# Performance work log

Hardware: AMD Instinct MI355X
Metric: run time of the kernel (lower is better)

Reference implementation:

```python
import jax, jax.numpy as jnp
import numpy as np

N = 100000
E = 3200000
IN_CH = 256
HID = 32
OUT_CH = 16


def setup_inputs() -> dict:
    key = jax.random.key(0)
    ks = jax.random.split(key, 9)
    x = jax.random.normal(ks[0], (N, IN_CH), dtype=jnp.float32)
    row = jax.random.randint(ks[1], (E,), 0, N)
    col = jax.random.randint(ks[2], (E,), 0, N)
    edge_index = jnp.stack([row, col], axis=0)  # [2, E]
    # Glorot-style init for GCN weights, zero bias (PyG default)
    def glorot(k, fan_in, fan_out):
        s = jnp.sqrt(6.0 / (fan_in + fan_out))
        return jax.random.uniform(k, (fan_in, fan_out), jnp.float32, -s, s)
    W1 = glorot(ks[3], IN_CH, HID)
    b1 = jnp.zeros((HID,), jnp.float32)
    W_mu = glorot(ks[4], HID, OUT_CH)
    b_mu = jnp.zeros((OUT_CH,), jnp.float32)
    W_lv = glorot(ks[5], HID, OUT_CH)
    b_lv = jnp.zeros((OUT_CH,), jnp.float32)
    return {"x": x, "edge_index": edge_index, "W1": W1, "b1": b1,
            "W_mu": W_mu, "b_mu": b_mu, "W_lv": W_lv, "b_lv": b_lv}


def _gcn_norm(edge_index, n):
    # PyG gcn_norm with add_self_loops=True: deg over target col including self-loop
    row, col = edge_index[0], edge_index[1]
    deg = jax.ops.segment_sum(jnp.ones((edge_index.shape[1],), jnp.float32), col,
                              num_segments=n) + 1.0  # +1 for self-loop
    dis = jax.lax.rsqrt(deg)  # deg >= 1 always
    edge_norm = dis[row] * dis[col]          # [E]
    self_norm = dis * dis                    # [N], norm of self-loop edge
    return edge_norm, self_norm


def _gcn_conv(x, W, b, row, col, edge_norm, self_norm, n):
    h = x @ W  # [N, F_out] — transform BEFORE aggregation (small F_out)
    agg = jax.ops.segment_sum(h[row] * edge_norm[:, None], col, num_segments=n)
    return agg + self_norm[:, None] * h + b


def reference(x, edge_index, W1, b1, W_mu, b_mu, W_lv, b_lv):
    n = x.shape[0]
    row, col = edge_index[0], edge_index[1]
    edge_norm, self_norm = _gcn_norm(edge_index, n)
    h = jax.nn.relu(_gcn_conv(x, W1, b1, row, col, edge_norm, self_norm, n))
    mu = _gcn_conv(h, W_mu, b_mu, row, col, edge_norm, self_norm, n)
    logvar = _gcn_conv(h, W_lv, b_lv, row, col, edge_norm, self_norm, n)
    return (mu, logvar)
```

## Files before the change

kernel.cpp:

```cpp
#include <hip/hip_runtime.h>

#define N_NODES 100000
#define E_EDGES 3200000
#define IN_CH 256
#define HID 32
#define OUT_CH 16

#define B_BUCKETS 250
#define NPB 400
#define CAP 20000
#define PB 256
#define PCH (E_EDGES / PB)
#define GEMM_BLOCKS ((N_NODES + 63) / 64)

typedef unsigned short u16;
typedef __attribute__((ext_vector_type(8))) short bf16x8;
typedef __attribute__((ext_vector_type(4))) float f32x4;

__device__ __forceinline__ unsigned bf16rtn(float f) {
    unsigned u = __float_as_uint(f);
    return (u + 0x7FFFu + ((u >> 16) & 1u)) >> 16;
}
__device__ __forceinline__ float bflo(unsigned u) { return __uint_as_float(u << 16); }
__device__ __forceinline__ float bfhi(unsigned u) { return __uint_as_float(u & 0xFFFF0000u); }


__global__ __launch_bounds__(256) void k_pre(const int* __restrict__ col,
                                             int* __restrict__ ghist,
                                             const float* __restrict__ W1,
                                             const float* __restrict__ x,
                                             u16* __restrict__ h0sh, int e, int n) {
    int bid = blockIdx.x;
    int tid = threadIdx.x;
    if (bid < PB) {
        __shared__ int h[B_BUCKETS];
        for (int i = tid; i < B_BUCKETS; i += 256) h[i] = 0;
        __syncthreads();
        int lo = bid * PCH, hi = lo + PCH;
        for (int i = lo + tid; i < hi; i += 256)
            atomicAdd(&h[col[i] / NPB], 1);
        __syncthreads();
        for (int i = tid; i < B_BUCKETS; i += 256)
            ghist[bid * B_BUCKETS + i] = h[i];
    } else {
        int gbid = bid - PB;
        int lane = tid & 63;
        int wv = tid >> 6;
        int vbase = gbid * 64 + wv * 16;
        if (vbase >= n) return;
        int arow = lane & 15;
        int kg = lane >> 4;
        const float* xr = x + (size_t)(vbase + arow) * IN_CH + kg * 8;

        uint4 bfrag[8][2];
        int colc0 = lane & 15;
        int krow0 = (lane >> 4) * 8;
#pragma unroll
        for (int kt = 0; kt < 8; ++kt) {
#pragma unroll
            for (int ct = 0; ct < 2; ++ct) {
                const float* wp = W1 + (size_t)(kt * 32 + krow0) * HID + ct * 16 + colc0;
                unsigned p[4];
#pragma unroll
                for (int pp = 0; pp < 4; ++pp) {
                    unsigned lo = bf16rtn(wp[(2 * pp) * HID]);
                    unsigned hi = bf16rtn(wp[(2 * pp + 1) * HID]);
                    p[pp] = lo | (hi << 16);
                }
                bfrag[kt][ct] = make_uint4(p[0], p[1], p[2], p[3]);
            }
        }

        f32x4 acc0 = {0.f, 0.f, 0.f, 0.f};
        f32x4 acc1 = {0.f, 0.f, 0.f, 0.f};
#pragma unroll
        for (int kt = 0; kt < 8; ++kt) {
            float4 a0 = *reinterpret_cast<const float4*>(xr + kt * 32);
            float4 a1 = *reinterpret_cast<const float4*>(xr + kt * 32 + 4);
            union { unsigned u[4]; bf16x8 v; } af;
            af.u[0] = bf16rtn(a0.x) | (bf16rtn(a0.y) << 16);
            af.u[1] = bf16rtn(a0.z) | (bf16rtn(a0.w) << 16);
            af.u[2] = bf16rtn(a1.x) | (bf16rtn(a1.y) << 16);
            af.u[3] = bf16rtn(a1.z) | (bf16rtn(a1.w) << 16);
            union { uint4 q; bf16x8 v; } b0, b1;
            b0.q = bfrag[kt][0];
            b1.q = bfrag[kt][1];
            acc0 = __builtin_amdgcn_mfma_f32_16x16x32_bf16(af.v, b0.v, acc0, 0, 0, 0);
            acc1 = __builtin_amdgcn_mfma_f32_16x16x32_bf16(af.v, b1.v, acc1, 0, 0, 0);
        }

        int r0 = (lane >> 4) * 4;
        int colo = lane & 15;
#pragma unroll
        for (int r = 0; r < 4; ++r) {
            int v = vbase + r0 + r;
            h0sh[(size_t)v * HID + colo]      = (u16)bf16rtn(acc0[r]);
            h0sh[(size_t)v * HID + 16 + colo] = (u16)bf16rtn(acc1[r]);
        }
    }
}


__global__ __launch_bounds__(256) void k_scan(int* __restrict__ ghist, int* __restrict__ bcnt) {
    __shared__ int a[256], b[256];
    int bu = blockIdx.x, t = threadIdx.x;
    int v = ghist[t * B_BUCKETS + bu];
    a[t] = v;
    __syncthreads();
    int* sp = a; int* dp = b;
    for (int off = 1; off < 256; off <<= 1) {
        dp[t] = sp[t] + ((t >= off) ? sp[t - off] : 0);
        __syncthreads();
        int* tm = sp; sp = dp; dp = tm;
    }
    ghist[t * B_BUCKETS + bu] = sp[t] - v;
    if (t == 255) bcnt[bu] = sp[t];
}


__global__ void k_bscan(const int* __restrict__ bcnt, int* __restrict__ bstart) {
    __shared__ int a[256], b[256];
    int t = threadIdx.x;
    int myc = (t < B_BUCKETS) ? bcnt[t] : 0;
    a[t] = myc;
    __syncthreads();
    int* sp = a; int* dp = b;
    for (int off = 1; off < 256; off <<= 1) {
        dp[t] = sp[t] + ((t >= off) ? sp[t - off] : 0);
        __syncthreads();
        int* tm = sp; sp = dp; dp = tm;
    }
    int incl = sp[t];
    if (t < B_BUCKETS) bstart[t] = incl - myc;
    if (t == B_BUCKETS - 1) bstart[B_BUCKETS] = incl;
}


__global__ __launch_bounds__(256) void k_place(const int* __restrict__ row,
                                               const int* __restrict__ col,
                                               const int* __restrict__ bstart,
                                               const int* __restrict__ ghist,
                                               const int* __restrict__ bcnt,
                                               unsigned* __restrict__ psrc) {
    __shared__ unsigned stage[PCH];
    __shared__ unsigned char bb[PCH];
    __shared__ int base[B_BUCKETS];
    __shared__ int lstart[B_BUCKETS];
    __shared__ int cur[B_BUCKETS];
    __shared__ int sa[256], sb[256];
    int bid = blockIdx.x;
    int tid = threadIdx.x;

    int h = 0;
    if (tid < B_BUCKETS) {
        int e0 = ghist[bid * B_BUCKETS + tid];
        int e1 = (bid < PB - 1) ? ghist[(bid + 1) * B_BUCKETS + tid] : bcnt[tid];
        base[tid] = bstart[tid] + e0;
        h = e1 - e0;
    }
    sa[tid] = h;
    __syncthreads();
    int* sp = sa; int* dp = sb;
    for (int off = 1; off < 256; off <<= 1) {
        dp[tid] = sp[tid] + ((tid >= off) ? sp[tid - off] : 0);
        __syncthreads();
        int* tm = sp; sp = dp; dp = tm;
    }
    int ex = sp[tid] - h;
    if (tid < B_BUCKETS) { lstart[tid] = ex; cur[tid] = ex; }
    __syncthreads();

    int lo = bid * PCH;
    for (int i = lo + tid; i < lo + PCH; i += 256) {
        int c = col[i];
        int b = c / NPB;
        int pos = atomicAdd(&cur[b], 1);
        stage[pos] = ((unsigned)(c - b * NPB) << 17) | (unsigned)row[i];
        bb[pos] = (unsigned char)b;
    }
    __syncthreads();

    for (int idx = tid; idx < PCH; idx += 256) {
        int b = bb[idx];
        psrc[base[b] + (idx - lstart[b])] = stage[idx];
    }
}


__global__ __launch_bounds__(512) void k_bsort(const unsigned* __restrict__ psrc,
                                               const int* __restrict__ bstart,
                                               int* __restrict__ srow, int* __restrict__ deg,
                                               int* __restrict__ start, float* __restrict__ dis,
                                               u16* __restrict__ h0sh) {
    __shared__ unsigned buf[CAP];
    __shared__ int cnt[512];
    __shared__ int sa[512];
    __shared__ int sb[512];
    int b = blockIdx.x, t = threadIdx.x;
    int s0 = bstart[b], s1 = bstart[b + 1], len = s1 - s0;

    cnt[t] = 0;
    __syncthreads();
    for (int i = t; i < len; i += 512)
        atomicAdd(&cnt[psrc[s0 + i] >> 17], 1);
    __syncthreads();

    sa[t] = cnt[t];
    __syncthreads();
    int* sp = sa; int* dp = sb;
    for (int off = 1; off < 512; off <<= 1) {
        dp[t] = sp[t] + ((t >= off) ? sp[t - off] : 0);
        __syncthreads();
        int* tm = sp; sp = dp; dp = tm;
    }
    int ex = sp[t] - cnt[t];
    __syncthreads();
    sa[t] = ex;
    sb[t] = ex;
    float dvv = 0.f;
    if (t < NPB) {
        int node = b * NPB + t;
        int d = cnt[t];
        deg[node] = d;
        start[node] = s0 + ex;
        dvv = rsqrtf((float)(d + 1));
        dis[node] = dvv;
    }
    __syncthreads();

    bool fits = (len <= CAP);
    for (int i = t; i < len; i += 512) {
        unsigned p = psrc[s0 + i];
        int cl = (int)(p >> 17);
        int pos = atomicAdd(&sb[cl], 1);
        if (fits) buf[pos] = p & 0x1FFFFu;
        else      srow[s0 + pos] = (int)(p & 0x1FFFFu);
    }
    __syncthreads();
    if (fits)
        for (int i = t; i < len; i += 512)
            srow[s0 + i] = (int)buf[i];

    if (t < NPB) {
        int node = b * NPB + t;
        uint4* p4 = reinterpret_cast<uint4*>(h0sh + (size_t)node * HID);
#pragma unroll
        for (int qq = 0; qq < 4; ++qq) {
            uint4 pv = p4[qq];
            unsigned r[4];
            unsigned comp[4] = {pv.x, pv.y, pv.z, pv.w};
#pragma unroll
            for (int k = 0; k < 4; ++k) {
                float lo = bflo(comp[k]) * dvv;
                float hi = bfhi(comp[k]) * dvv;
                r[k] = bf16rtn(lo) | (bf16rtn(hi) << 16);
            }
            p4[qq] = make_uint4(r[0], r[1], r[2], r[3]);
        }
    }
}

#define ACC8(gv)                                   \
    acc[0] += bflo(gv.x); acc[1] += bfhi(gv.x);    \
    acc[2] += bflo(gv.y); acc[3] += bfhi(gv.y);    \
    acc[4] += bflo(gv.z); acc[5] += bfhi(gv.z);    \
    acc[6] += bflo(gv.w); acc[7] += bfhi(gv.w);

#define GATHER16(TAB)                                                                            \
    for (; i + 16 <= d; i += 16) {                                                               \
        int u0 = srow[s+i+0], u1 = srow[s+i+1], u2 = srow[s+i+2], u3 = srow[s+i+3];              \
        int u4 = srow[s+i+4], u5 = srow[s+i+5], u6 = srow[s+i+6], u7 = srow[s+i+7];              \
        int u8 = srow[s+i+8], u9 = srow[s+i+9], ua = srow[s+i+10], ub = srow[s+i+11];            \
        int uc = srow[s+i+12], ud = srow[s+i+13], ue = srow[s+i+14], uf = srow[s+i+15];          \
        uint4 g0 = *reinterpret_cast<const uint4*>(TAB + (size_t)u0 * HID + q * 8);              \
        uint4 g1 = *reinterpret_cast<const uint4*>(TAB + (size_t)u1 * HID + q * 8);              \
        uint4 g2 = *reinterpret_cast<const uint4*>(TAB + (size_t)u2 * HID + q * 8);              \
        uint4 g3 = *reinterpret_cast<const uint4*>(TAB + (size_t)u3 * HID + q * 8);              \
        uint4 g4 = *reinterpret_cast<const uint4*>(TAB + (size_t)u4 * HID + q * 8);              \
        uint4 g5 = *reinterpret_cast<const uint4*>(TAB + (size_t)u5 * HID + q * 8);              \
        uint4 g6 = *reinterpret_cast<const uint4*>(TAB + (size_t)u6 * HID + q * 8);              \
        uint4 g7 = *reinterpret_cast<const uint4*>(TAB + (size_t)u7 * HID + q * 8);              \
        uint4 g8 = *reinterpret_cast<const uint4*>(TAB + (size_t)u8 * HID + q * 8);              \
        uint4 g9 = *reinterpret_cast<const uint4*>(TAB + (size_t)u9 * HID + q * 8);              \
        uint4 ga = *reinterpret_cast<const uint4*>(TAB + (size_t)ua * HID + q * 8);              \
        uint4 gb = *reinterpret_cast<const uint4*>(TAB + (size_t)ub * HID + q * 8);              \
        uint4 gc = *reinterpret_cast<const uint4*>(TAB + (size_t)uc * HID + q * 8);              \
        uint4 gd = *reinterpret_cast<const uint4*>(TAB + (size_t)ud * HID + q * 8);              \
        uint4 ge = *reinterpret_cast<const uint4*>(TAB + (size_t)ue * HID + q * 8);              \
        uint4 gf = *reinterpret_cast<const uint4*>(TAB + (size_t)uf * HID + q * 8);              \
        ACC8(g0) ACC8(g1) ACC8(g2) ACC8(g3) ACC8(g4) ACC8(g5) ACC8(g6) ACC8(g7)                  \
        ACC8(g8) ACC8(g9) ACC8(ga) ACC8(gb) ACC8(gc) ACC8(gd) ACC8(ge) ACC8(gf)                  \
    }                                                                                            \
    for (; i + 8 <= d; i += 8) {                                                                 \
        int u0 = srow[s+i+0], u1 = srow[s+i+1], u2 = srow[s+i+2], u3 = srow[s+i+3];              \
        int u4 = srow[s+i+4], u5 = srow[s+i+5], u6 = srow[s+i+6], u7 = srow[s+i+7];              \
        uint4 g0 = *reinterpret_cast<const uint4*>(TAB + (size_t)u0 * HID + q * 8);              \
        uint4 g1 = *reinterpret_cast<const uint4*>(TAB + (size_t)u1 * HID + q * 8);              \
        uint4 g2 = *reinterpret_cast<const uint4*>(TAB + (size_t)u2 * HID + q * 8);              \
        uint4 g3 = *reinterpret_cast<const uint4*>(TAB + (size_t)u3 * HID + q * 8);              \
        uint4 g4 = *reinterpret_cast<const uint4*>(TAB + (size_t)u4 * HID + q * 8);              \
        uint4 g5 = *reinterpret_cast<const uint4*>(TAB + (size_t)u5 * HID + q * 8);              \
        uint4 g6 = *reinterpret_cast<const uint4*>(TAB + (size_t)u6 * HID + q * 8);              \
        uint4 g7 = *reinterpret_cast<const uint4*>(TAB + (size_t)u7 * HID + q * 8);              \
        ACC8(g0) ACC8(g1) ACC8(g2) ACC8(g3) ACC8(g4) ACC8(g5) ACC8(g6) ACC8(g7)                  \
    }                                                                                            \
    for (; i < d; ++i) {                                                                         \
        int u = srow[s + i];                                                                     \
        uint4 gv = *reinterpret_cast<const uint4*>(TAB + (size_t)u * HID + q * 8);               \
        ACC8(gv)                                                                                 \
    }


__global__ __launch_bounds__(256, 4) void k_agg1(const u16* __restrict__ h0sh,
                                                 const int* __restrict__ srow,
                                                 const int* __restrict__ start,
                                                 const int* __restrict__ deg,
                                                 const float* __restrict__ dis,
                                                 const float* __restrict__ b1,
                                                 u16* __restrict__ hsh, int n) {
    int tid = threadIdx.x;
    int lane = tid & 63;
    int g = lane >> 2;
    int q = lane & 3;
    int wv = tid >> 6;
    int v = blockIdx.x * 64 + wv * 16 + g;
    if (v >= n) v = n - 1;
    int s = start[v], d = deg[v];
    float dv = dis[v];

    float acc[8];
#pragma unroll
    for (int c = 0; c < 8; ++c) acc[c] = 0.f;

    int i = 0;
    GATHER16(h0sh)

    uint4 sv = *reinterpret_cast<const uint4*>(h0sh + (size_t)v * HID + q * 8);
    float self[8] = {bflo(sv.x), bfhi(sv.x), bflo(sv.y), bfhi(sv.y),
                     bflo(sv.z), bfhi(sv.z), bflo(sv.w), bfhi(sv.w)};
    float4 ba = *reinterpret_cast<const float4*>(b1 + q * 8);
    float4 bb = *reinterpret_cast<const float4*>(b1 + q * 8 + 4);
    float bias[8] = {ba.x, ba.y, ba.z, ba.w, bb.x, bb.y, bb.z, bb.w};

    unsigned pk[4];
#pragma unroll
    for (int p = 0; p < 4; ++p) {
        float o0 = dv * fmaxf(0.f, fmaf(dv, acc[2 * p] + self[2 * p], bias[2 * p]));
        float o1 = dv * fmaxf(0.f, fmaf(dv, acc[2 * p + 1] + self[2 * p + 1], bias[2 * p + 1]));
        pk[p] = bf16rtn(o0) | (bf16rtn(o1) << 16);
    }
    *reinterpret_cast<uint4*>(hsh + (size_t)v * HID + q * 8) = make_uint4(pk[0], pk[1], pk[2], pk[3]);
}


__global__ __launch_bounds__(256, 4) void k_agg2(const u16* __restrict__ hsh,
                                                 const int* __restrict__ srow,
                                                 const int* __restrict__ start,
                                                 const int* __restrict__ deg,
                                                 const float* __restrict__ dis,
                                                 const float* __restrict__ Wmu,
                                                 const float* __restrict__ Wlv,
                                                 const float* __restrict__ bmu,
                                                 const float* __restrict__ blv,
                                                 float* __restrict__ out, int n) {
    __shared__ float wc[32][33];
    __shared__ float svec[64][33];
    int tid = threadIdx.x;
    for (int i2 = tid; i2 < 32 * 32; i2 += 256) {
        int k = i2 >> 5, c = i2 & 31;
        wc[k][c] = (c < OUT_CH) ? Wmu[k * OUT_CH + c] : Wlv[k * OUT_CH + (c - OUT_CH)];
    }

    int lane = tid & 63;
    int g = lane >> 2;
    int q = lane & 3;
    int wv = tid >> 6;
    int dd = wv * 16 + g;
    int v = blockIdx.x * 64 + dd;
    if (v >= n) v = n - 1;
    int s = start[v], d = deg[v];
    float dv = dis[v];

    float acc[8];
#pragma unroll
    for (int c = 0; c < 8; ++c) acc[c] = 0.f;

    int i = 0;
    GATHER16(hsh)

    uint4 sv4 = *reinterpret_cast<const uint4*>(hsh + (size_t)v * HID + q * 8);
    float self[8] = {bflo(sv4.x), bfhi(sv4.x), bflo(sv4.y), bfhi(sv4.y),
                     bflo(sv4.z), bfhi(sv4.z), bflo(sv4.w), bfhi(sv4.w)};
#pragma unroll
    for (int c = 0; c < 8; ++c)
        svec[dd][q * 8 + c] = dv * (acc[c] + self[c]);
    __syncthreads();

    int dd2 = tid >> 2;
    int oo = tid & 3;
    int v2 = blockIdx.x * 64 + dd2;
    if (v2 >= n) return;
    float o[8];
#pragma unroll
    for (int c = 0; c < 8; ++c) o[c] = 0.f;
#pragma unroll 8
    for (int k = 0; k < 32; ++k) {
        float skv = svec[dd2][k];
        const float* wr = &wc[k][oo * 8];
        o[0] = fmaf(skv, wr[0], o[0]);
        o[1] = fmaf(skv, wr[1], o[1]);
        o[2] = fmaf(skv, wr[2], o[2]);
        o[3] = fmaf(skv, wr[3], o[3]);
        o[4] = fmaf(skv, wr[4], o[4]);
        o[5] = fmaf(skv, wr[5], o[5]);
        o[6] = fmaf(skv, wr[6], o[6]);
        o[7] = fmaf(skv, wr[7], o[7]);
    }
    float* dst;
    const float* bsrc;
    if (oo < 2) { dst = out + (size_t)v2 * OUT_CH + oo * 8;                       bsrc = bmu + oo * 8; }
    else        { dst = out + (size_t)N_NODES * OUT_CH + (size_t)v2 * OUT_CH + (oo - 2) * 8; bsrc = blv + (oo - 2) * 8; }
    float4 b0 = *reinterpret_cast<const float4*>(bsrc);
    float4 b1v = *reinterpret_cast<const float4*>(bsrc + 4);
    *reinterpret_cast<float4*>(dst)     = make_float4(o[0] + b0.x, o[1] + b0.y, o[2] + b0.z, o[3] + b0.w);
    *reinterpret_cast<float4*>(dst + 4) = make_float4(o[4] + b1v.x, o[5] + b1v.y, o[6] + b1v.z, o[7] + b1v.w);
}


extern "C" void kernel_launch(void* const* d_in, const int* in_sizes, int n_in,
                              void* d_out, int out_size, void* d_ws, size_t ws_size,
                              hipStream_t stream) {
    const float* x   = (const float*)d_in[0];
    const int*   ei  = (const int*)d_in[1];
    const float* W1  = (const float*)d_in[2];
    const float* b1  = (const float*)d_in[3];
    const float* Wmu = (const float*)d_in[4];
    const float* bmu = (const float*)d_in[5];
    const float* Wlv = (const float*)d_in[6];
    const float* blv = (const float*)d_in[7];
    float* out = (float*)d_out;

    const int* row = ei;
    const int* col = ei + E_EDGES;

    char* w = (char*)d_ws;
    int*   bcnt   = (int*)w;  w += 1024;
    int*   bstart = (int*)w;  w += 1024;
    int*   ghist  = (int*)w;  w += (size_t)PB * B_BUCKETS * 4;
    int*   deg    = (int*)w;  w += (size_t)N_NODES * 4;
    float* dis    = (float*)w; w += (size_t)N_NODES * 4;
    int*   start  = (int*)w;  w += (size_t)N_NODES * 4;
    int*   srow   = (int*)w;  w += (size_t)E_EDGES * 4;
    u16*   h0sh   = (u16*)w;  w += (size_t)N_NODES * HID * 2;
    u16*   hsh    = (u16*)w;  w += (size_t)N_NODES * HID * 2;
    unsigned* psrc = (unsigned*)w; w += (size_t)E_EDGES * 4;

    const int TB = 256;
    k_pre<<<PB + GEMM_BLOCKS, TB, 0, stream>>>(col, ghist, W1, x, h0sh, E_EDGES, N_NODES);
    k_scan<<<B_BUCKETS, 256, 0, stream>>>(ghist, bcnt);
    k_bscan<<<1, 256, 0, stream>>>(bcnt, bstart);
    k_place<<<PB, TB, 0, stream>>>(row, col, bstart, ghist, bcnt, psrc);
    k_bsort<<<B_BUCKETS, 512, 0, stream>>>(psrc, bstart, srow, deg, start, dis, h0sh);
    k_agg1<<<(N_NODES + 63) / 64, TB, 0, stream>>>(h0sh, srow, start, deg, dis, b1, hsh, N_NODES);
    k_agg2<<<(N_NODES + 63) / 64, TB, 0, stream>>>(hsh, srow, start, deg, dis,
                                                   Wmu, Wlv, bmu, blv, out, N_NODES);
}
```

Measured before the change: 170.5 us.

## Pad per-node CSR neighbor lists to multiples of 16 with zero sentinel row

Each node's neighbor list in srow is padded to a multiple of 16 and aligned, with padding entries pointing to an extra all-zero row appended to both feature tables. The gather loops then read indices as int4 vectors and drop the 8-wide and scalar tail loops. k_bsort also stops staging sorted edges in a large shared-memory buffer and scatters directly to global memory. This cuts tail-loop divergence and scalar index loads, at the cost of extra wasted gathers (about 7.5 padded entries per node on average) and uncoalesced scattered writes in the sort kernel.

```diff
diff --git a/kernel.cpp b/kernel.cpp
--- a/kernel.cpp
+++ b/kernel.cpp
@@ -8,10 +8,10 @@
 
 #define B_BUCKETS 250
 #define NPB 400
-#define CAP 20000
 #define PB 256
 #define PCH (E_EDGES / PB)
 #define GEMM_BLOCKS ((N_NODES + 63) / 64)
+#define PADSTRIDE 6416
 
 typedef unsigned short u16;
 typedef __attribute__((ext_vector_type(8))) short bf16x8;
@@ -118,9 +118,14 @@
 }
 
 
-__global__ void k_bscan(const int* __restrict__ bcnt, int* __restrict__ bstart) {
+__global__ void k_bscan(const int* __restrict__ bcnt, int* __restrict__ bstart,
+                        u16* __restrict__ h0sh, u16* __restrict__ hsh) {
     __shared__ int a[256], b[256];
     int t = threadIdx.x;
+    if (t < HID) {
+        h0sh[(size_t)N_NODES * HID + t] = 0;
+        hsh[(size_t)N_NODES * HID + t] = 0;
+    }
     int myc = (t < B_BUCKETS) ? bcnt[t] : 0;
     a[t] = myc;
     __syncthreads();
@@ -192,12 +197,13 @@
                                                int* __restrict__ srow, int* __restrict__ deg,
                                                int* __restrict__ start, float* __restrict__ dis,
                                                u16* __restrict__ h0sh) {
-    __shared__ unsigned buf[CAP];
     __shared__ int cnt[512];
     __shared__ int sa[512];
     __shared__ int sb[512];
+    __shared__ int cur[512];
     int b = blockIdx.x, t = threadIdx.x;
     int s0 = bstart[b], s1 = bstart[b + 1], len = s1 - s0;
+    int pbase = ((s0 + 15) & ~15) + b * PADSTRIDE;
 
     cnt[t] = 0;
     __syncthreads();
@@ -205,7 +211,9 @@
         atomicAdd(&cnt[psrc[s0 + i] >> 17], 1);
     __syncthreads();
 
-    sa[t] = cnt[t];
+    int d = cnt[t];
+    int dpad = (d + 15) & ~15;
+    sa[t] = dpad;
     __syncthreads();
     int* sp = sa; int* dp = sb;
     for (int off = 1; off < 512; off <<= 1) {
@@ -213,33 +221,28 @@
         __syncthreads();
         int* tm = sp; sp = dp; dp = tm;
     }
-    int ex = sp[t] - cnt[t];
-    __syncthreads();
-    sa[t] = ex;
-    sb[t] = ex;
+    int pex = sp[t] - dpad;
+    __syncthreads();
+    int gstart = pbase + pex;
+    cur[t] = gstart;
     float dvv = 0.f;
     if (t < NPB) {
         int node = b * NPB + t;
-        int d = cnt[t];
         deg[node] = d;
-        start[node] = s0 + ex;
+        start[node] = gstart;
         dvv = rsqrtf((float)(d + 1));
         dis[node] = dvv;
-    }
-    __syncthreads();
-
-    bool fits = (len <= CAP);
+        for (int j = d; j < dpad; ++j)
+            srow[gstart + j] = N_NODES;
+    }
+    __syncthreads();
+
     for (int i = t; i < len; i += 512) {
         unsigned p = psrc[s0 + i];
         int cl = (int)(p >> 17);
-        int pos = atomicAdd(&sb[cl], 1);
-        if (fits) buf[pos] = p & 0x1FFFFu;
-        else      srow[s0 + pos] = (int)(p & 0x1FFFFu);
-    }
-    __syncthreads();
-    if (fits)
-        for (int i = t; i < len; i += 512)
-            srow[s0 + i] = (int)buf[i];
+        int pos = atomicAdd(&cur[cl], 1);
+        srow[pos] = (int)(p & 0x1FFFFu);
+    }
 
     if (t < NPB) {
         int node = b * NPB + t;
@@ -266,48 +269,30 @@
     acc[4] += bflo(gv.z); acc[5] += bfhi(gv.z);    \
     acc[6] += bflo(gv.w); acc[7] += bfhi(gv.w);
 
-#define GATHER16(TAB)                                                                            \
-    for (; i + 16 <= d; i += 16) {                                                               \
-        int u0 = srow[s+i+0], u1 = srow[s+i+1], u2 = srow[s+i+2], u3 = srow[s+i+3];              \
-        int u4 = srow[s+i+4], u5 = srow[s+i+5], u6 = srow[s+i+6], u7 = srow[s+i+7];              \
-        int u8 = srow[s+i+8], u9 = srow[s+i+9], ua = srow[s+i+10], ub = srow[s+i+11];            \
-        int uc = srow[s+i+12], ud = srow[s+i+13], ue = srow[s+i+14], uf = srow[s+i+15];          \
-        uint4 g0 = *reinterpret_cast<const uint4*>(TAB + (size_t)u0 * HID + q * 8);              \
-        uint4 g1 = *reinterpret_cast<const uint4*>(TAB + (size_t)u1 * HID + q * 8);              \
-        uint4 g2 = *reinterpret_cast<const uint4*>(TAB + (size_t)u2 * HID + q * 8);              \
-        uint4 g3 = *reinterpret_cast<const uint4*>(TAB + (size_t)u3 * HID + q * 8);              \
-        uint4 g4 = *reinterpret_cast<const uint4*>(TAB + (size_t)u4 * HID + q * 8);              \
-        uint4 g5 = *reinterpret_cast<const uint4*>(TAB + (size_t)u5 * HID + q * 8);              \
-        uint4 g6 = *reinterpret_cast<const uint4*>(TAB + (size_t)u6 * HID + q * 8);              \
-        uint4 g7 = *reinterpret_cast<const uint4*>(TAB + (size_t)u7 * HID + q * 8);              \
-        uint4 g8 = *reinterpret_cast<const uint4*>(TAB + (size_t)u8 * HID + q * 8);              \
-        uint4 g9 = *reinterpret_cast<const uint4*>(TAB + (size_t)u9 * HID + q * 8);              \
-        uint4 ga = *reinterpret_cast<const uint4*>(TAB + (size_t)ua * HID + q * 8);              \
-        uint4 gb = *reinterpret_cast<const uint4*>(TAB + (size_t)ub * HID + q * 8);              \
-        uint4 gc = *reinterpret_cast<const uint4*>(TAB + (size_t)uc * HID + q * 8);              \
-        uint4 gd = *reinterpret_cast<const uint4*>(TAB + (size_t)ud * HID + q * 8);              \
-        uint4 ge = *reinterpret_cast<const uint4*>(TAB + (size_t)ue * HID + q * 8);              \
-        uint4 gf = *reinterpret_cast<const uint4*>(TAB + (size_t)uf * HID + q * 8);              \
+#define GATHER16V(TAB)                                                                           \
+    for (int i = 0; i < dpad; i += 16) {                                                         \
+        int4 ui0 = *reinterpret_cast<const int4*>(srow + s + i);                                 \
+        int4 ui1 = *reinterpret_cast<const int4*>(srow + s + i + 4);                             \
+        int4 ui2 = *reinterpret_cast<const int4*>(srow + s + i + 8);                             \
+        int4 ui3 = *reinterpret_cast<const int4*>(srow + s + i + 12);                            \
+        uint4 g0 = *reinterpret_cast<const uint4*>(TAB + (size_t)ui0.x * HID + q * 8);           \
+        uint4 g1 = *reinterpret_cast<const uint4*>(TAB + (size_t)ui0.y * HID + q * 8);           \
+        uint4 g2 = *reinterpret_cast<const uint4*>(TAB + (size_t)ui0.z * HID + q * 8);           \
+        uint4 g3 = *reinterpret_cast<const uint4*>(TAB + (size_t)ui0.w * HID + q * 8);           \
+        uint4 g4 = *reinterpret_cast<const uint4*>(TAB + (size_t)ui1.x * HID + q * 8);           \
+        uint4 g5 = *reinterpret_cast<const uint4*>(TAB + (size_t)ui1.y * HID + q * 8);           \
+        uint4 g6 = *reinterpret_cast<const uint4*>(TAB + (size_t)ui1.z * HID + q * 8);           \
+        uint4 g7 = *reinterpret_cast<const uint4*>(TAB + (size_t)ui1.w * HID + q * 8);           \
+        uint4 g8 = *reinterpret_cast<const uint4*>(TAB + (size_t)ui2.x * HID + q * 8);           \
+        uint4 g9 = *reinterpret_cast<const uint4*>(TAB + (size_t)ui2.y * HID + q * 8);           \
+        uint4 ga = *reinterpret_cast<const uint4*>(TAB + (size_t)ui2.z * HID + q * 8);           \
+        uint4 gb = *reinterpret_cast<const uint4*>(TAB + (size_t)ui2.w * HID + q * 8);           \
+        uint4 gc = *reinterpret_cast<const uint4*>(TAB + (size_t)ui3.x * HID + q * 8);           \
+        uint4 gd = *reinterpret_cast<const uint4*>(TAB + (size_t)ui3.y * HID + q * 8);           \
+        uint4 ge = *reinterpret_cast<const uint4*>(TAB + (size_t)ui3.z * HID + q * 8);           \
+        uint4 gf = *reinterpret_cast<const uint4*>(TAB + (size_t)ui3.w * HID + q * 8);           \
         ACC8(g0) ACC8(g1) ACC8(g2) ACC8(g3) ACC8(g4) ACC8(g5) ACC8(g6) ACC8(g7)                  \
         ACC8(g8) ACC8(g9) ACC8(ga) ACC8(gb) ACC8(gc) ACC8(gd) ACC8(ge) ACC8(gf)                  \
-    }                                                                                            \
-    for (; i + 8 <= d; i += 8) {                                                                 \
-        int u0 = srow[s+i+0], u1 = srow[s+i+1], u2 = srow[s+i+2], u3 = srow[s+i+3];              \
-        int u4 = srow[s+i+4], u5 = srow[s+i+5], u6 = srow[s+i+6], u7 = srow[s+i+7];              \
-        uint4 g0 = *reinterpret_cast<const uint4*>(TAB + (size_t)u0 * HID + q * 8);              \
-        uint4 g1 = *reinterpret_cast<const uint4*>(TAB + (size_t)u1 * HID + q * 8);              \
-        uint4 g2 = *reinterpret_cast<const uint4*>(TAB + (size_t)u2 * HID + q * 8);              \
-        uint4 g3 = *reinterpret_cast<const uint4*>(TAB + (size_t)u3 * HID + q * 8);              \
-        uint4 g4 = *reinterpret_cast<const uint4*>(TAB + (size_t)u4 * HID + q * 8);              \
-        uint4 g5 = *reinterpret_cast<const uint4*>(TAB + (size_t)u5 * HID + q * 8);              \
-        uint4 g6 = *reinterpret_cast<const uint4*>(TAB + (size_t)u6 * HID + q * 8);              \
-        uint4 g7 = *reinterpret_cast<const uint4*>(TAB + (size_t)u7 * HID + q * 8);              \
-        ACC8(g0) ACC8(g1) ACC8(g2) ACC8(g3) ACC8(g4) ACC8(g5) ACC8(g6) ACC8(g7)                  \
-    }                                                                                            \
-    for (; i < d; ++i) {                                                                         \
-        int u = srow[s + i];                                                                     \
-        uint4 gv = *reinterpret_cast<const uint4*>(TAB + (size_t)u * HID + q * 8);               \
-        ACC8(gv)                                                                                 \
     }
 
 
@@ -325,15 +310,15 @@
     int wv = tid >> 6;
     int v = blockIdx.x * 64 + wv * 16 + g;
     if (v >= n) v = n - 1;
-    int s = start[v], d = deg[v];
+    int s = start[v];
+    int dpad = (deg[v] + 15) & ~15;
     float dv = dis[v];
 
     float acc[8];
 #pragma unroll
     for (int c = 0; c < 8; ++c) acc[c] = 0.f;
 
-    int i = 0;
-    GATHER16(h0sh)
+    GATHER16V(h0sh)
 
     uint4 sv = *reinterpret_cast<const uint4*>(h0sh + (size_t)v * HID + q * 8);
     float self[8] = {bflo(sv.x), bfhi(sv.x), bflo(sv.y), bfhi(sv.y),
@@ -378,15 +363,15 @@
     int dd = wv * 16 + g;
     int v = blockIdx.x * 64 + dd;
     if (v >= n) v = n - 1;
-    int s = start[v], d = deg[v];
+    int s = start[v];
+    int dpad = (deg[v] + 15) & ~15;
     float dv = dis[v];
 
     float acc[8];
 #pragma unroll
     for (int c = 0; c < 8; ++c) acc[c] = 0.f;
 
-    int i = 0;
-    GATHER16(hsh)
+    GATHER16V(hsh)
 
     uint4 sv4 = *reinterpret_cast<const uint4*>(hsh + (size_t)v * HID + q * 8);
     float self[8] = {bflo(sv4.x), bfhi(sv4.x), bflo(sv4.y), bfhi(sv4.y),
@@ -450,15 +435,15 @@
     int*   deg    = (int*)w;  w += (size_t)N_NODES * 4;
     float* dis    = (float*)w; w += (size_t)N_NODES * 4;
     int*   start  = (int*)w;  w += (size_t)N_NODES * 4;
-    int*   srow   = (int*)w;  w += (size_t)E_EDGES * 4;
-    u16*   h0sh   = (u16*)w;  w += (size_t)N_NODES * HID * 2;
-    u16*   hsh    = (u16*)w;  w += (size_t)N_NODES * HID * 2;
+    int*   srow   = (int*)w;  w += (size_t)(E_EDGES + 16 + B_BUCKETS * PADSTRIDE) * 4;
+    u16*   h0sh   = (u16*)w;  w += (size_t)(N_NODES + 1) * HID * 2;
+    u16*   hsh    = (u16*)w;  w += (size_t)(N_NODES + 1) * HID * 2;
     unsigned* psrc = (unsigned*)w; w += (size_t)E_EDGES * 4;
 
     const int TB = 256;
     k_pre<<<PB + GEMM_BLOCKS, TB, 0, stream>>>(col, ghist, W1, x, h0sh, E_EDGES, N_NODES);
     k_scan<<<B_BUCKETS, 256, 0, stream>>>(ghist, bcnt);
-    k_bscan<<<1, 256, 0, stream>>>(bcnt, bstart);
+    k_bscan<<<1, 256, 0, stream>>>(bcnt, bstart, h0sh, hsh);
     k_place<<<PB, TB, 0, stream>>>(row, col, bstart, ghist, bcnt, psrc);
     k_bsort<<<B_BUCKETS, 512, 0, stream>>>(psrc, bstart, srow, deg, start, dis, h0sh);
     k_agg1<<<(N_NODES + 63) / 64, TB, 0, stream>>>(h0sh, srow, start, deg, dis, b1, hsh, N_NODES);
```

New measurement: 169.7 us. No clear change (-0.5%).
